# Kernel tuning notes

Measured on AMD Instinct MI355X. Metric: run time of the kernel, lower is better.

## Reference

```python
import jax, jax.numpy as jnp
import numpy as np

N = 50000
E = 800000
IN_DIM = 128
HID = 128
HEADS = 8
OUT_DIM = 64
NEG_SLOPE = 0.2


def setup_inputs() -> dict:
    key = jax.random.key(0)
    ks = jax.random.split(key, 12)
    x = jax.random.normal(ks[0], (N, IN_DIM), dtype=jnp.float32)
    edge_index = jax.random.randint(ks[1], (2, E), 0, N, dtype=jnp.int64)
    C1 = HID // HEADS  # per-head out dim of layer 1
    s1 = 1.0 / np.sqrt(IN_DIM)
    s2 = 1.0 / np.sqrt(HID)
    W1 = jax.random.uniform(ks[2], (IN_DIM, HEADS * C1), jnp.float32, -s1, s1)
    a_src1 = jax.random.uniform(ks[3], (HEADS, C1), jnp.float32, -1.0, 1.0)
    a_dst1 = jax.random.uniform(ks[4], (HEADS, C1), jnp.float32, -1.0, 1.0)
    b1 = jnp.zeros((HEADS * C1,), jnp.float32)
    W2 = jax.random.uniform(ks[5], (HID, OUT_DIM), jnp.float32, -s2, s2)
    a_src2 = jax.random.uniform(ks[6], (1, OUT_DIM), jnp.float32, -1.0, 1.0)
    a_dst2 = jax.random.uniform(ks[7], (1, OUT_DIM), jnp.float32, -1.0, 1.0)
    b2 = jnp.zeros((OUT_DIM,), jnp.float32)
    return {"x": x, "edge_index": edge_index, "W1": W1, "a_src1": a_src1,
            "a_dst1": a_dst1, "b1": b1, "W2": W2, "a_src2": a_src2,
            "a_dst2": a_dst2, "b2": b2}


def gat_conv(x, src, dst, W, a_s, a_d, b, n_heads, c_head):
    # Linear projection per head: [N, H, C]
    h = (x @ W).reshape(N, n_heads, c_head)
    # Per-node attention terms: [N, H]
    alpha_s = jnp.einsum('nhc,hc->nh', h, a_s)
    alpha_d = jnp.einsum('nhc,hc->nh', h, a_d)
    # Per-edge raw scores: [Etot, H]
    score = jax.nn.leaky_relu(alpha_s[src] + alpha_d[dst], negative_slope=NEG_SLOPE)
    # Segment softmax over edges sharing the same destination
    m = jax.ops.segment_max(score, dst, num_segments=N)
    e = jnp.exp(score - m[dst])
    denom = jax.ops.segment_sum(e, dst, num_segments=N)
    alpha = e / denom[dst]  # every node has a self-loop -> denom > 0
    # Weighted aggregation: scatter-add alpha * h_src into destinations
    out = jax.ops.segment_sum(alpha[:, :, None] * h[src], dst, num_segments=N)
    return out.reshape(N, n_heads * c_head) + b


def reference(x, edge_index, W1, a_src1, a_dst1, b1, W2, a_src2, a_dst2, b2):
    # add self loops (GATConv add_self_loops=True)
    loops = jnp.arange(N, dtype=edge_index.dtype)
    src = jnp.concatenate([edge_index[0], loops])
    dst = jnp.concatenate([edge_index[1], loops])
    C1 = HID // HEADS
    h = gat_conv(x, src, dst, W1, a_src1, a_dst1, b1, HEADS, C1)
    h = jax.nn.elu(h)  # dropout = 0 (eval)
    out = gat_conv(h, src, dst, W2, a_src2, a_dst2, b2, 1, OUT_DIM)
    return jax.nn.log_softmax(out, axis=-1)
```

## Files before the change

### kernel.cpp

```cpp
#include <hip/hip_runtime.h>
#include <math.h>

typedef unsigned int  u32;
typedef unsigned short u16;
typedef short bf16x8 __attribute__((ext_vector_type(8)));
typedef float f32x4  __attribute__((ext_vector_type(4)));

#define NN    50000
#define NE    800000
#define ET    (NE + NN)
#define IND   128
#define HIDD  128
#define NH    8
#define OD    64
#define SLOPE 0.2f

#define NB    196
#define EPB   4096
#define NBB   ((NE + EPB - 1) / EPB)
#define LCAP  64
#define CAPB  5120
#define CPAD  16
#define BSTRIDE 7168

#define W1EXT 144
#define W2EXT 80
#define WPB   112
#define G1B   391

__device__ __forceinline__ u32 bf16rne(float f) {
    u32 u = __float_as_uint(f);
    return (u + 0x7fffu + ((u >> 16) & 1u)) >> 16;
}

#define LR(s) fmaxf((s), SLOPE * (s))

__global__ __launch_bounds__(256) void k_prep_bin(
    const int* __restrict__ ei, int* __restrict__ cnt, u32* __restrict__ staging,
    const float* __restrict__ W1, const float* __restrict__ W2,
    const float* __restrict__ as1w, const float* __restrict__ ad1w,
    const float* __restrict__ as2w, const float* __restrict__ ad2w,
    u16* __restrict__ Wt1, u16* __restrict__ Wt2,
    u32* __restrict__ h1b, float* __restrict__ as1, float* __restrict__ as2)
{
    __shared__ u32 lbuf[NB * LCAP];
    __shared__ int lcnt[NB];
    __shared__ int gbase[NB];
    const int t = threadIdx.x;

    if (blockIdx.x >= NBB) {
        const int i = (blockIdx.x - NBB) * 256 + t;
        if (i < 64) h1b[(size_t)64 * NN + i] = 0;
        if (i < 8)  as1[(size_t)NH * NN + i] = -1e30f;
        if (i == 8) as2[NN] = -1e30f;

        if (i < W1EXT * 128) {
            const int j = i >> 7, k = i & 127;
            float v;
            if (j < 128) {
                v = W1[k * 128 + j];
            } else if (j < 136) {
                const int h = j - 128;
                v = 0.f;
                for (int c = 0; c < 16; ++c)
                    v += W1[k * 128 + h * 16 + c] * as1w[h * 16 + c];
            } else {
                const int h = j - 136;
                v = 0.f;
                for (int c = 0; c < 16; ++c)
                    v += W1[k * 128 + h * 16 + c] * ad1w[h * 16 + c];
            }
            Wt1[j * 128 + k] = (u16)bf16rne(v);
        } else if (i < W1EXT * 128 + W2EXT * 128) {
            const int i2 = i - W1EXT * 128;
            const int j = i2 >> 7, k = i2 & 127;
            float v = 0.f;
            if (j < 64) {
                v = W2[k * 64 + j];
            } else if (j == 64) {
                for (int c = 0; c < 64; ++c) v += W2[k * 64 + c] * as2w[c];
            } else if (j == 65) {
                for (int c = 0; c < 64; ++c) v += W2[k * 64 + c] * ad2w[c];
            }
            Wt2[j * 128 + k] = (u16)bf16rne(v);
        }
        return;
    }

    const int e0 = blockIdx.x * EPB;
    for (int i = t; i < NB; i += 256) lcnt[i] = 0;
    __syncthreads();

    for (int i = t; i < EPB; i += 256) {
        const int e = e0 + i;
        if (e >= NE) break;
        const int src = ei[e];
        const int dst = ei[NE + e];
        const int b = dst >> 8;
        const int p = atomicAdd(&lcnt[b], 1);
        lbuf[b * LCAP + p] = ((u32)(dst & 255) << 16) | (u32)src;
    }
    __syncthreads();

    for (int i = t; i < NB; i += 256)
        gbase[i] = atomicAdd(&cnt[i * CPAD], lcnt[i]);
    __syncthreads();

    for (int b = t; b < NB; b += 256) {
        const int n = lcnt[b];
        const int gb = gbase[b];
        u32* dstp = staging + (size_t)b * CAPB + gb;
        const u32* srcp = lbuf + b * LCAP;
        for (int j = 0; j < n; ++j) dstp[j] = srcp[j];
    }
}

__global__ __launch_bounds__(512) void k_place_gemm1(
    const int* __restrict__ cnt, const u32* __restrict__ staging,
    int* __restrict__ rowptr, int* __restrict__ rowend,
    u16* __restrict__ sorted16,
    const float* __restrict__ x, const u16* __restrict__ Wt1,
    u16* __restrict__ h1s, float* __restrict__ as1, float* __restrict__ ad1)
{
    __shared__ u32 xb[128 * 64];
    __shared__ u32 Wb[W1EXT * 64];
    const int tid = threadIdx.x;

    if (blockIdx.x < NB) {
        int* hist = (int*)xb;
        int* cur  = hist + 256;
        int* scan = cur + 256;
        const int b = blockIdx.x;
        const int tot = cnt[b * CPAD];
        const int base = b * BSTRIDE;

        if (tid < 256) hist[tid] = ((b * 256 + tid) < NN) ? 1 : 0;
        __syncthreads();

        for (int i = tid; i < tot; i += 512)
            atomicAdd(&hist[staging[(size_t)b * CAPB + i] >> 16], 1);
        __syncthreads();

        if (tid < 256) scan[tid] = (hist[tid] + 7) & ~7;
        __syncthreads();
        for (int off = 1; off < 256; off <<= 1) {
            int v = 0;
            if (tid < 256 && tid >= off) v = scan[tid - off];
            __syncthreads();
            if (tid < 256) scan[tid] += v;
            __syncthreads();
        }
        if (tid < 256) {
            const int padded = (hist[tid] + 7) & ~7;
            const int excl = (tid == 0) ? 0 : scan[tid - 1];
            const int node = b * 256 + tid;
            if (node < NN) {
                rowptr[node] = base + excl;
                rowend[node] = base + excl + padded;
                sorted16[base + excl] = (u16)node;
                for (int j = hist[tid]; j < padded; ++j)
                    sorted16[base + excl + j] = (u16)NN;
                cur[tid] = excl + 1;
            } else {
                cur[tid] = excl;
            }
        }
        __syncthreads();
        for (int i = tid; i < tot; i += 512) {
            const u32 v = staging[(size_t)b * CAPB + i];
            const int pos = atomicAdd(&cur[v >> 16], 1);
            sorted16[base + pos] = (u16)(v & 0xffffu);
        }
        return;
    }

    const int row0 = (blockIdx.x - NB) * 128;

    {
        const uint4* Wt = (const uint4*)Wt1;
        for (int p = 0; p < 5; ++p) {
            const int id = p * 512 + tid;
            if (id < W1EXT * 16) {
                const int n = id >> 4, c = id & 15;
                *(uint4*)(Wb + n * 64 + ((c ^ (n & 15)) << 2)) = Wt[n * 16 + c];
            }
        }
    }
    for (int p = 0; p < 4; ++p) {
        const int id = p * 512 + tid;
        const int m = id >> 4, c = id & 15;
        const int row = row0 + m;
        uint4 v = make_uint4(0, 0, 0, 0);
        if (row < NN) {
            const float4 f0 = *(const float4*)(x + (size_t)row * 128 + c * 8);
            const float4 f1 = *(const float4*)(x + (size_t)row * 128 + c * 8 + 4);
            v.x = bf16rne(f0.x) | (bf16rne(f0.y) << 16);
            v.y = bf16rne(f0.z) | (bf16rne(f0.w) << 16);
            v.z = bf16rne(f1.x) | (bf16rne(f1.y) << 16);
            v.w = bf16rne(f1.z) | (bf16rne(f1.w) << 16);
        }
        *(uint4*)(xb + m * 64 + ((c ^ (m & 15)) << 2)) = v;
    }
    __syncthreads();

    const int w = tid >> 6, lane = tid & 63;
    const int nl = lane & 15, quad = lane >> 4;
    f32x4 acc[9] = {};
    for (int kk = 0; kk < 4; ++kk) {
        const int cm = kk * 4 + quad;
        const bf16x8 a = *(const bf16x8*)(xb + (16 * w + nl) * 64 + ((cm ^ nl) << 2));
#pragma unroll
        for (int tn = 0; tn < 9; ++tn) {
            const bf16x8 b = *(const bf16x8*)(Wb + (16 * tn + nl) * 64 + ((cm ^ nl) << 2));
            acc[tn] = __builtin_amdgcn_mfma_f32_16x16x32_bf16(a, b, acc[tn], 0, 0, 0);
        }
    }

    __syncthreads();
    {
        u16* h1ld = (u16*)xb;
#pragma unroll
        for (int tn = 0; tn < 8; ++tn) {
#pragma unroll
            for (int r = 0; r < 4; ++r) {
                const int row = 16 * w + quad * 4 + r;
                h1ld[row * 128 + 16 * tn + nl] = (u16)bf16rne(acc[tn][r]);
            }
        }
    }
#pragma unroll
    for (int r = 0; r < 4; ++r) {
        const int row = row0 + 16 * w + quad * 4 + r;
        if (row < NN) {
            const float v = acc[8][r];
            if (nl < 8) as1[row * NH + nl] = v;
            else        ad1[row * NH + (nl - 8)] = v;
        }
    }
    __syncthreads();
    for (int p = 0; p < 4; ++p) {
        const int id = p * 512 + tid;
        const int row = id >> 4, c = id & 15;
        const int grow = row0 + row;
        if (grow < NN)
            ((uint4*)h1s)[(size_t)grow * 16 + c] = ((const uint4*)xb)[row * 16 + c];
    }
}

__global__ __launch_bounds__(512) void k_gemm2(
    const u32* __restrict__ act2b, const u16* __restrict__ Wt2,
    u16* __restrict__ h2s, float* __restrict__ as2, float* __restrict__ ad2)
{
    __shared__ u32 xb[128 * 64];
    __shared__ u32 Wb[W2EXT * 64];
    const int tid = threadIdx.x;
    const int row0 = blockIdx.x * 128;

    {
        const uint4* Wt = (const uint4*)Wt2;
        for (int p = 0; p < 3; ++p) {
            const int id = p * 512 + tid;
            if (id < W2EXT * 16) {
                const int n = id >> 4, c = id & 15;
                *(uint4*)(Wb + n * 64 + ((c ^ (n & 15)) << 2)) = Wt[n * 16 + c];
            }
        }
    }
    for (int p = 0; p < 4; ++p) {
        const int id = p * 512 + tid;
        const int m = id >> 4, c = id & 15;
        const int row = row0 + m;
        uint4 v = make_uint4(0, 0, 0, 0);
        if (row < NN) v = ((const uint4*)act2b)[(size_t)row * 16 + c];
        *(uint4*)(xb + m * 64 + ((c ^ (m & 15)) << 2)) = v;
    }
    __syncthreads();

    const int w = tid >> 6, lane = tid & 63;
    const int nl = lane & 15, quad = lane >> 4;
    f32x4 acc[5] = {};
    for (int kk = 0; kk < 4; ++kk) {
        const int cm = kk * 4 + quad;
        const bf16x8 a = *(const bf16x8*)(xb + (16 * w + nl) * 64 + ((cm ^ nl) << 2));
#pragma unroll
        for (int tn = 0; tn < 5; ++tn) {
            const bf16x8 b = *(const bf16x8*)(Wb + (16 * tn + nl) * 64 + ((cm ^ nl) << 2));
            acc[tn] = __builtin_amdgcn_mfma_f32_16x16x32_bf16(a, b, acc[tn], 0, 0, 0);
        }
    }

    __syncthreads();
    {
        u16* h2ld = (u16*)xb;
#pragma unroll
        for (int tn = 0; tn < 4; ++tn) {
#pragma unroll
            for (int r = 0; r < 4; ++r) {
                const int row = 16 * w + quad * 4 + r;
                h2ld[row * 64 + 16 * tn + nl] = (u16)bf16rne(acc[tn][r]);
            }
        }
    }
#pragma unroll
    for (int r = 0; r < 4; ++r) {
        const int row = row0 + 16 * w + quad * 4 + r;
        if (row < NN) {
            const float v = acc[4][r];
            if (nl == 0) as2[row] = v;
            else if (nl == 1) ad2[row] = v;
        }
    }
    __syncthreads();
    for (int p = 0; p < 2; ++p) {
        const int id = p * 512 + tid;
        const int row = id >> 3, c = id & 7;
        const int grow = row0 + row;
        if (grow < NN)
            ((uint4*)h2s)[(size_t)grow * 8 + c] = ((const uint4*)xb)[row * 8 + c];
    }
}

#define PG1(KK, S, G, WJ) do {                                                \
    const uint4 p = *(const uint4*)(sorted16 + (KK));                         \
    S[0] = p.x & 0xffffu; S[1] = p.x >> 16;                                   \
    S[2] = p.y & 0xffffu; S[3] = p.y >> 16;                                   \
    S[4] = p.z & 0xffffu; S[5] = p.z >> 16;                                   \
    S[6] = p.w & 0xffffu; S[7] = p.w >> 16;                                   \
    const u32 hlf = (head & 4) ? ((head & 2) ? p.w : p.z)                     \
                               : ((head & 2) ? p.y : p.x);                    \
    const u32 sj = (head & 1) ? (hlf >> 16) : (hlf & 0xffffu);                \
    WJ = __expf(LR(as1[sj * NH + eh] + adeh));                                \
    _Pragma("unroll") for (int j = 0; j < 8; ++j)                             \
        G[j] = h1b[S[j] * 64 + lane];                                         \
} while (0)

#define CONS1(G, WJ) do {                                                     \
    _Pragma("unroll") for (int j = 0; j < 8; ++j) {                           \
        const float wv = __uint_as_float((u32)__builtin_amdgcn_ds_bpermute(   \
            h4 + j * 32, (int)__float_as_uint(WJ)));                          \
        acc0 += wv * __uint_as_float(G[j] << 16);                             \
        acc1 += wv * __uint_as_float(G[j] & 0xffff0000u);                     \
        den  += wv; }                                                         \
} while (0)

__global__ __launch_bounds__(256) void k_agg1(
    const int* __restrict__ rowptr, const int* __restrict__ rowend,
    const u16* __restrict__ sorted16,
    const u32* __restrict__ h1b, const float* __restrict__ as1,
    const float* __restrict__ ad1,
    u32* __restrict__ act2b)
{
    const int node = blockIdx.x * 4 + (threadIdx.x >> 6);
    const int lane = threadIdx.x & 63;
    const int head = lane >> 3;
    const int eh   = lane & 7;
    const float adeh = ad1[node * NH + eh];
    const int k0 = rowptr[node], kend = rowend[node];
    const int h4 = head << 2;
    float acc0 = 0.f, acc1 = 0.f, den = 0.f;
    u32 sA[8], gA[8], sB[8], gB[8];
    float wA, wB;

    PG1(k0, sA, gA, wA);
    int k = k0 + 8;
    while (k + 16 <= kend) {
        PG1(k, sB, gB, wB);      CONS1(gA, wA);
        PG1(k + 8, sA, gA, wA);  CONS1(gB, wB);
        k += 16;
    }
    if (k < kend) {
        PG1(k, sB, gB, wB);  CONS1(gA, wA);  CONS1(gB, wB);
    } else {
        CONS1(gA, wA);
    }

    const float inv = 1.f / den;
    float v0 = acc0 * inv, v1 = acc1 * inv;
    v0 = v0 > 0.f ? v0 : expm1f(v0);
    v1 = v1 > 0.f ? v1 : expm1f(v1);
    act2b[node * 64 + lane] = bf16rne(v0) | (bf16rne(v1) << 16);
}

#define PG2(KK, S, G, WJ) do {                                                \
    const uint4 p = *(const uint4*)(sorted16 + (KK));                         \
    S[0] = p.x & 0xffffu; S[1] = p.x >> 16;                                   \
    S[2] = p.y & 0xffffu; S[3] = p.y >> 16;                                   \
    S[4] = p.z & 0xffffu; S[5] = p.z >> 16;                                   \
    S[6] = p.w & 0xffffu; S[7] = p.w >> 16;                                   \
    const u32 hlf = (lane & 4) ? ((lane & 2) ? p.w : p.z)                     \
                               : ((lane & 2) ? p.y : p.x);                    \
    const u32 sj = (lane & 1) ? (hlf >> 16) : (hlf & 0xffffu);                \
    WJ = __expf(LR(as2[sj] + adv));                                           \
    _Pragma("unroll") for (int j = 0; j < 8; ++j)                             \
        G[j] = h2s[S[j] * 64 + lane];                                         \
} while (0)

#define CONS2(G, WJ) do {                                                     \
    _Pragma("unroll") for (int j = 0; j < 8; ++j) {                           \
        const float wv = __uint_as_float((u32)__builtin_amdgcn_ds_bpermute(   \
            j << 2, (int)__float_as_uint(WJ)));                               \
        acc += wv * __uint_as_float(((u32)G[j]) << 16);                       \
        den += wv; }                                                          \
} while (0)

__global__ __launch_bounds__(256) void k_agg2(
    const int* __restrict__ rowptr, const int* __restrict__ rowend,
    const u16* __restrict__ sorted16,
    const u16* __restrict__ h2s, const float* __restrict__ as2,
    const float* __restrict__ ad2,
    float* __restrict__ out)
{
    const int node = blockIdx.x * 4 + (threadIdx.x >> 6);
    const int lane = threadIdx.x & 63;
    const float adv = ad2[node];
    const int k0 = rowptr[node], kend = rowend[node];
    float acc = 0.f, den = 0.f;
    u32 sA[8], gA[8], sB[8], gB[8];
    float wA, wB;

    PG2(k0, sA, gA, wA);
    int k = k0 + 8;
    while (k + 16 <= kend) {
        PG2(k, sB, gB, wB);      CONS2(gA, wA);
        PG2(k + 8, sA, gA, wA);  CONS2(gB, wB);
        k += 16;
    }
    if (k < kend) {
        PG2(k, sB, gB, wB);  CONS2(gA, wA);  CONS2(gB, wB);
    } else {
        CONS2(gA, wA);
    }

    const float v = acc / den;
    float m = v;
    for (int kk = 1; kk < 64; kk <<= 1) m = fmaxf(m, __shfl_xor(m, kk));
    float se = __expf(v - m);
    for (int kk = 1; kk < 64; kk <<= 1) se += __shfl_xor(se, kk);
    out[node * 64 + lane] = v - m - logf(se);
}

extern "C" void kernel_launch(void* const* d_in, const int* in_sizes, int n_in,
                              void* d_out, int out_size, void* d_ws, size_t ws_size,
                              hipStream_t stream)
{
    (void)in_sizes; (void)n_in; (void)out_size; (void)ws_size;
    const float* x    = (const float*)d_in[0];
    const int*   ei   = (const int*)d_in[1];
    const float* W1   = (const float*)d_in[2];
    const float* as1w = (const float*)d_in[3];
    const float* ad1w = (const float*)d_in[4];
    const float* W2   = (const float*)d_in[6];
    const float* as2w = (const float*)d_in[7];
    const float* ad2w = (const float*)d_in[8];
    float* out = (float*)d_out;

    u32* ws = (u32*)d_ws;
    size_t o = 0;
    auto take = [&](size_t n) { size_t r = o; o += (n + 15) & ~(size_t)15; return r; };

    u32*   h1b      = ws + take((size_t)64 * (NN + 1));
    float* as1      = (float*)(ws + take((size_t)NH * NN + 8));
    float* ad1      = (float*)(ws + take((size_t)NH * NN));
    u32*   act2b    = ws + take((size_t)64 * NN);
    float* as2      = (float*)(ws + take(NN + 1));
    float* ad2      = (float*)(ws + take(NN));
    int*   rowptr   = (int*)(ws + take(NN));
    int*   rowend   = (int*)(ws + take(NN));
    u16*   sorted16 = (u16*)(ws + take(((size_t)NB * BSTRIDE + 1) / 2));
    u32*   staging  = ws + take((size_t)NB * CAPB);
    int*   cnt      = (int*)(ws + take(NB * CPAD));
    u16*   Wt1      = (u16*)(ws + take((size_t)W1EXT * 128 / 2));
    u16*   Wt2      = (u16*)(ws + take((size_t)W2EXT * 128 / 2));
    u16*   h1s      = (u16*)h1b;
    u16*   h2s      = (u16*)h1b;

    hipMemsetAsync(cnt, 0, NB * CPAD * sizeof(int), stream);

    k_prep_bin<<<NBB + WPB, 256, 0, stream>>>(
        ei, cnt, staging, W1, W2, as1w, ad1w, as2w, ad2w,
        Wt1, Wt2, h1b, as1, as2);

    k_place_gemm1<<<NB + G1B, 512, 0, stream>>>(
        cnt, staging, rowptr, rowend, sorted16, x, Wt1, h1s, as1, ad1);

    k_agg1<<<NN / 4, 256, 0, stream>>>(rowptr, rowend, sorted16, h1b, as1, ad1, act2b);
    k_gemm2<<<G1B, 512, 0, stream>>>(act2b, Wt2, h2s, as2, ad2);
    k_agg2<<<NN / 4, 256, 0, stream>>>(rowptr, rowend, sorted16, h2s, as2, ad2, out);
}
```

Before: 183.5 us.

## Gather feature rows with 16-byte vector loads split across lane groups in aggregation

Both aggregation kernels change how source feature rows are gathered. Before, each lane loaded one 32-bit word per edge for eight edges. Now each lane loads a 16-byte chunk of a row, so one wavefront gathers several edges' rows at once (2 edges per pass in layer 1, 8 in layer 2). Partial sums are then combined across lane groups with xor-shuffles, and the output is written by a subset of lanes using vector stores. The aim is fewer, wider memory instructions and fewer bpermutes per edge, at the cost of extra cross-lane reductions and more accumulator registers.

```diff
diff --git a/kernel.cpp b/kernel.cpp
--- a/kernel.cpp
+++ b/kernel.cpp
@@ -34,6 +34,13 @@
 }
 
 #define LR(s) fmaxf((s), SLOPE * (s))
+
+__device__ __forceinline__ u32 sel8(uint4 p, int e) {
+    const u32 c = (e & 4) ? ((e & 2) ? p.w : p.z) : ((e & 2) ? p.y : p.x);
+    return (e & 1) ? (c >> 16) : (c & 0xffffu);
+}
+#define BFLO(u) __uint_as_float((u) << 16)
+#define BFHI(u) __uint_as_float((u) & 0xffff0000u)
 
 __global__ __launch_bounds__(256) void k_prep_bin(
     const int* __restrict__ ei, int* __restrict__ cnt, u32* __restrict__ staging,
@@ -320,33 +327,36 @@
     }
 }
 
-#define PG1(KK, S, G, WJ) do {                                                \
-    const uint4 p = *(const uint4*)(sorted16 + (KK));                         \
-    S[0] = p.x & 0xffffu; S[1] = p.x >> 16;                                   \
-    S[2] = p.y & 0xffffu; S[3] = p.y >> 16;                                   \
-    S[4] = p.z & 0xffffu; S[5] = p.z >> 16;                                   \
-    S[6] = p.w & 0xffffu; S[7] = p.w >> 16;                                   \
-    const u32 hlf = (head & 4) ? ((head & 2) ? p.w : p.z)                     \
-                               : ((head & 2) ? p.y : p.x);                    \
-    const u32 sj = (head & 1) ? (hlf >> 16) : (hlf & 0xffffu);                \
+#define PG1(KK, P, G0, G1, WJ) do {                                           \
+    P = *(const uint4*)(sorted16 + (KK));                                     \
+    const u32 sj = sel8(P, head);                                             \
     WJ = __expf(LR(as1[sj * NH + eh] + adeh));                                \
-    _Pragma("unroll") for (int j = 0; j < 8; ++j)                             \
-        G[j] = h1b[S[j] * 64 + lane];                                         \
+    const u32 s0 = sel8(P, esel);                                             \
+    const u32 s1 = sel8(P, 4 + esel);                                         \
+    G0 = *(const uint4*)(h1g + (size_t)s0 * 128 + ch8);                       \
+    G1 = *(const uint4*)(h1g + (size_t)s1 * 128 + ch8);                       \
 } while (0)
 
-#define CONS1(G, WJ) do {                                                     \
-    _Pragma("unroll") for (int j = 0; j < 8; ++j) {                           \
-        const float wv = __uint_as_float((u32)__builtin_amdgcn_ds_bpermute(   \
-            h4 + j * 32, (int)__float_as_uint(WJ)));                          \
-        acc0 += wv * __uint_as_float(G[j] << 16);                             \
-        acc1 += wv * __uint_as_float(G[j] & 0xffff0000u);                     \
-        den  += wv; }                                                         \
+#define CONS1(G0, G1, WJ) do {                                                \
+    const float w0 = __uint_as_float((u32)__builtin_amdgcn_ds_bpermute(       \
+        bp0, (int)__float_as_uint(WJ)));                                      \
+    const float w1 = __uint_as_float((u32)__builtin_amdgcn_ds_bpermute(       \
+        bp1, (int)__float_as_uint(WJ)));                                      \
+    acc[0] += w0 * BFLO(G0.x); acc[1] += w0 * BFHI(G0.x);                     \
+    acc[2] += w0 * BFLO(G0.y); acc[3] += w0 * BFHI(G0.y);                     \
+    acc[4] += w0 * BFLO(G0.z); acc[5] += w0 * BFHI(G0.z);                     \
+    acc[6] += w0 * BFLO(G0.w); acc[7] += w0 * BFHI(G0.w);                     \
+    acc[0] += w1 * BFLO(G1.x); acc[1] += w1 * BFHI(G1.x);                     \
+    acc[2] += w1 * BFLO(G1.y); acc[3] += w1 * BFHI(G1.y);                     \
+    acc[4] += w1 * BFLO(G1.z); acc[5] += w1 * BFHI(G1.z);                     \
+    acc[6] += w1 * BFLO(G1.w); acc[7] += w1 * BFHI(G1.w);                     \
+    den += w0 + w1;                                                           \
 } while (0)
 
 __global__ __launch_bounds__(256) void k_agg1(
     const int* __restrict__ rowptr, const int* __restrict__ rowend,
     const u16* __restrict__ sorted16,
-    const u32* __restrict__ h1b, const float* __restrict__ as1,
+    const u16* __restrict__ h1g, const float* __restrict__ as1,
     const float* __restrict__ ad1,
     u32* __restrict__ act2b)
 {
@@ -355,88 +365,134 @@
     const int head = lane >> 3;
     const int eh   = lane & 7;
     const float adeh = ad1[node * NH + eh];
+    const int esel = lane >> 4;
+    const int ch8  = (lane & 15) * 8;
+    const int mh   = (lane & 15) >> 1;
+    const int bp0  = (esel * 8 + mh) << 2;
+    const int bp1  = bp0 + 128;
     const int k0 = rowptr[node], kend = rowend[node];
-    const int h4 = head << 2;
-    float acc0 = 0.f, acc1 = 0.f, den = 0.f;
-    u32 sA[8], gA[8], sB[8], gB[8];
+    float acc[8] = {0.f, 0.f, 0.f, 0.f, 0.f, 0.f, 0.f, 0.f};
+    float den = 0.f;
+    uint4 pA, gA0, gA1, pB, gB0, gB1;
     float wA, wB;
 
-    PG1(k0, sA, gA, wA);
+    PG1(k0, pA, gA0, gA1, wA);
     int k = k0 + 8;
     while (k + 16 <= kend) {
-        PG1(k, sB, gB, wB);      CONS1(gA, wA);
-        PG1(k + 8, sA, gA, wA);  CONS1(gB, wB);
+        PG1(k, pB, gB0, gB1, wB);        CONS1(gA0, gA1, wA);
+        PG1(k + 8, pA, gA0, gA1, wA);    CONS1(gB0, gB1, wB);
         k += 16;
     }
     if (k < kend) {
-        PG1(k, sB, gB, wB);  CONS1(gA, wA);  CONS1(gB, wB);
+        PG1(k, pB, gB0, gB1, wB);  CONS1(gA0, gA1, wA);  CONS1(gB0, gB1, wB);
     } else {
-        CONS1(gA, wA);
-    }
+        CONS1(gA0, gA1, wA);
+    }
+
+#pragma unroll
+    for (int i = 0; i < 8; ++i) {
+        acc[i] += __shfl_xor(acc[i], 16);
+        acc[i] += __shfl_xor(acc[i], 32);
+    }
+    den += __shfl_xor(den, 16);
+    den += __shfl_xor(den, 32);
 
     const float inv = 1.f / den;
-    float v0 = acc0 * inv, v1 = acc1 * inv;
-    v0 = v0 > 0.f ? v0 : expm1f(v0);
-    v1 = v1 > 0.f ? v1 : expm1f(v1);
-    act2b[node * 64 + lane] = bf16rne(v0) | (bf16rne(v1) << 16);
-}
-
-#define PG2(KK, S, G, WJ) do {                                                \
-    const uint4 p = *(const uint4*)(sorted16 + (KK));                         \
-    S[0] = p.x & 0xffffu; S[1] = p.x >> 16;                                   \
-    S[2] = p.y & 0xffffu; S[3] = p.y >> 16;                                   \
-    S[4] = p.z & 0xffffu; S[5] = p.z >> 16;                                   \
-    S[6] = p.w & 0xffffu; S[7] = p.w >> 16;                                   \
-    const u32 hlf = (lane & 4) ? ((lane & 2) ? p.w : p.z)                     \
-                               : ((lane & 2) ? p.y : p.x);                    \
-    const u32 sj = (lane & 1) ? (hlf >> 16) : (hlf & 0xffffu);                \
+    u32 o[4];
+#pragma unroll
+    for (int i = 0; i < 4; ++i) {
+        float v0 = acc[2 * i] * inv, v1 = acc[2 * i + 1] * inv;
+        v0 = v0 > 0.f ? v0 : expm1f(v0);
+        v1 = v1 > 0.f ? v1 : expm1f(v1);
+        o[i] = bf16rne(v0) | (bf16rne(v1) << 16);
+    }
+    if (lane < 16)
+        *(uint4*)(act2b + (size_t)node * 64 + lane * 4) =
+            make_uint4(o[0], o[1], o[2], o[3]);
+}
+
+#define PG2(KK, P, G, WJ) do {                                                \
+    P = *(const uint4*)(sorted16 + (KK));                                     \
+    const u32 sj = sel8(P, eh2);                                              \
     WJ = __expf(LR(as2[sj] + adv));                                           \
-    _Pragma("unroll") for (int j = 0; j < 8; ++j)                             \
-        G[j] = h2s[S[j] * 64 + lane];                                         \
+    const u32 s = sel8(P, es2);                                               \
+    G = *(const uint4*)(h2g + (size_t)s * 64 + ch8b);                         \
 } while (0)
 
 #define CONS2(G, WJ) do {                                                     \
-    _Pragma("unroll") for (int j = 0; j < 8; ++j) {                           \
-        const float wv = __uint_as_float((u32)__builtin_amdgcn_ds_bpermute(   \
-            j << 2, (int)__float_as_uint(WJ)));                               \
-        acc += wv * __uint_as_float(((u32)G[j]) << 16);                       \
-        den += wv; }                                                          \
+    const float wv = __uint_as_float((u32)__builtin_amdgcn_ds_bpermute(       \
+        bpa, (int)__float_as_uint(WJ)));                                      \
+    acc[0] += wv * BFLO(G.x); acc[1] += wv * BFHI(G.x);                       \
+    acc[2] += wv * BFLO(G.y); acc[3] += wv * BFHI(G.y);                       \
+    acc[4] += wv * BFLO(G.z); acc[5] += wv * BFHI(G.z);                       \
+    acc[6] += wv * BFLO(G.w); acc[7] += wv * BFHI(G.w);                       \
+    den += wv;                                                                \
 } while (0)
 
 __global__ __launch_bounds__(256) void k_agg2(
     const int* __restrict__ rowptr, const int* __restrict__ rowend,
     const u16* __restrict__ sorted16,
-    const u16* __restrict__ h2s, const float* __restrict__ as2,
+    const u16* __restrict__ h2g, const float* __restrict__ as2,
     const float* __restrict__ ad2,
     float* __restrict__ out)
 {
     const int node = blockIdx.x * 4 + (threadIdx.x >> 6);
     const int lane = threadIdx.x & 63;
     const float adv = ad2[node];
+    const int eh2  = lane & 7;
+    const int es2  = lane >> 3;
+    const int ch8b = (lane & 7) * 8;
+    const int bpa  = es2 << 2;
     const int k0 = rowptr[node], kend = rowend[node];
-    float acc = 0.f, den = 0.f;
-    u32 sA[8], gA[8], sB[8], gB[8];
+    float acc[8] = {0.f, 0.f, 0.f, 0.f, 0.f, 0.f, 0.f, 0.f};
+    float den = 0.f;
+    uint4 pA, gA, pB, gB;
     float wA, wB;
 
-    PG2(k0, sA, gA, wA);
+    PG2(k0, pA, gA, wA);
     int k = k0 + 8;
     while (k + 16 <= kend) {
-        PG2(k, sB, gB, wB);      CONS2(gA, wA);
-        PG2(k + 8, sA, gA, wA);  CONS2(gB, wB);
+        PG2(k, pB, gB, wB);      CONS2(gA, wA);
+        PG2(k + 8, pA, gA, wA);  CONS2(gB, wB);
         k += 16;
     }
     if (k < kend) {
-        PG2(k, sB, gB, wB);  CONS2(gA, wA);  CONS2(gB, wB);
+        PG2(k, pB, gB, wB);  CONS2(gA, wA);  CONS2(gB, wB);
     } else {
         CONS2(gA, wA);
     }
 
-    const float v = acc / den;
-    float m = v;
-    for (int kk = 1; kk < 64; kk <<= 1) m = fmaxf(m, __shfl_xor(m, kk));
-    float se = __expf(v - m);
-    for (int kk = 1; kk < 64; kk <<= 1) se += __shfl_xor(se, kk);
-    out[node * 64 + lane] = v - m - logf(se);
+#pragma unroll
+    for (int i = 0; i < 8; ++i) {
+        acc[i] += __shfl_xor(acc[i], 8);
+        acc[i] += __shfl_xor(acc[i], 16);
+        acc[i] += __shfl_xor(acc[i], 32);
+    }
+    den += __shfl_xor(den, 8);
+    den += __shfl_xor(den, 16);
+    den += __shfl_xor(den, 32);
+
+    const float inv = 1.f / den;
+    float v[8];
+    float m = -1e30f;
+#pragma unroll
+    for (int i = 0; i < 8; ++i) { v[i] = acc[i] * inv; m = fmaxf(m, v[i]); }
+    m = fmaxf(m, __shfl_xor(m, 1));
+    m = fmaxf(m, __shfl_xor(m, 2));
+    m = fmaxf(m, __shfl_xor(m, 4));
+    float se = 0.f;
+#pragma unroll
+    for (int i = 0; i < 8; ++i) se += __expf(v[i] - m);
+    se += __shfl_xor(se, 1);
+    se += __shfl_xor(se, 2);
+    se += __shfl_xor(se, 4);
+    const float lse = m + logf(se);
+    if (lane < 8) {
+        float4 o0 = make_float4(v[0] - lse, v[1] - lse, v[2] - lse, v[3] - lse);
+        float4 o1 = make_float4(v[4] - lse, v[5] - lse, v[6] - lse, v[7] - lse);
+        *(float4*)(out + (size_t)node * 64 + lane * 8)     = o0;
+        *(float4*)(out + (size_t)node * 64 + lane * 8 + 4) = o1;
+    }
 }
 
 extern "C" void kernel_launch(void* const* d_in, const int* in_sizes, int n_in,
@@ -483,7 +539,7 @@
     k_place_gemm1<<<NB + G1B, 512, 0, stream>>>(
         cnt, staging, rowptr, rowend, sorted16, x, Wt1, h1s, as1, ad1);
 
-    k_agg1<<<NN / 4, 256, 0, stream>>>(rowptr, rowend, sorted16, h1b, as1, ad1, act2b);
+    k_agg1<<<NN / 4, 256, 0, stream>>>(rowptr, rowend, sorted16, h1s, as1, ad1, act2b);
     k_gemm2<<<G1B, 512, 0, stream>>>(act2b, Wt2, h2s, as2, ad2);
     k_agg2<<<NN / 4, 256, 0, stream>>>(rowptr, rowend, sorted16, h2s, as2, ad2, out);
 }
```

After: 190.3 us. +3.7%, slower.

## Split layer-1 features into head-pair slices for L2-local gather aggregation

Applied to the files above, without the earlier changes.

Stores layer-1 projected features and attention logits in four slice-major planes of two heads each. Aggregation then runs one block per node-quad per slice, so each block gathers a smaller working set. Each lane loads a 16-byte chunk for one of 16 edges and partial sums are reduced with cross-lane shuffles. Row padding grows to 16 entries to match the wider edge step. This aims to improve cache locality of the random gathers, at the cost of four times as many blocks, redundant index reads and extra padding work.

```diff
diff --git a/kernel.cpp b/kernel.cpp
--- a/kernel.cpp
+++ b/kernel.cpp
@@ -21,19 +21,30 @@
 #define LCAP  64
 #define CAPB  5120
 #define CPAD  16
-#define BSTRIDE 7168
+#define BSTRIDE 8192
 
 #define W1EXT 144
 #define W2EXT 80
 #define WPB   112
 #define G1B   391
 
+#define SL_ROW  16
+#define SL_STR  ((size_t)(NN + 1) * SL_ROW)
+#define PSTR    ((size_t)(NN + 1) * 2)
+
 __device__ __forceinline__ u32 bf16rne(float f) {
     u32 u = __float_as_uint(f);
     return (u + 0x7fffu + ((u >> 16) & 1u)) >> 16;
 }
 
 #define LR(s) fmaxf((s), SLOPE * (s))
+
+__device__ __forceinline__ u32 sel8(uint4 p, int e) {
+    const u32 c = (e & 4) ? ((e & 2) ? p.w : p.z) : ((e & 2) ? p.y : p.x);
+    return (e & 1) ? (c >> 16) : (c & 0xffffu);
+}
+#define BFLO(u) __uint_as_float((u) << 16)
+#define BFHI(u) __uint_as_float((u) & 0xffff0000u)
 
 __global__ __launch_bounds__(256) void k_prep_bin(
     const int* __restrict__ ei, int* __restrict__ cnt, u32* __restrict__ staging,
@@ -41,7 +52,7 @@
     const float* __restrict__ as1w, const float* __restrict__ ad1w,
     const float* __restrict__ as2w, const float* __restrict__ ad2w,
     u16* __restrict__ Wt1, u16* __restrict__ Wt2,
-    u32* __restrict__ h1b, float* __restrict__ as1, float* __restrict__ as2)
+    u32* __restrict__ h1sl, float* __restrict__ as1p, float* __restrict__ as2)
 {
     __shared__ u32 lbuf[NB * LCAP];
     __shared__ int lcnt[NB];
@@ -50,8 +61,10 @@
 
     if (blockIdx.x >= NBB) {
         const int i = (blockIdx.x - NBB) * 256 + t;
-        if (i < 64) h1b[(size_t)64 * NN + i] = 0;
-        if (i < 8)  as1[(size_t)NH * NN + i] = -1e30f;
+        if (i < 64)
+            h1sl[(size_t)(i >> 4) * SL_STR + (size_t)NN * SL_ROW + (i & 15)] = 0;
+        if (i < 8)
+            as1p[(size_t)(i >> 1) * PSTR + (size_t)NN * 2 + (i & 1)] = -1e30f;
         if (i == 8) as2[NN] = -1e30f;
 
         if (i < W1EXT * 128) {
@@ -120,7 +133,7 @@
     int* __restrict__ rowptr, int* __restrict__ rowend,
     u16* __restrict__ sorted16,
     const float* __restrict__ x, const u16* __restrict__ Wt1,
-    u16* __restrict__ h1s, float* __restrict__ as1, float* __restrict__ ad1)
+    u32* __restrict__ h1sl, float* __restrict__ as1p, float* __restrict__ ad1p)
 {
     __shared__ u32 xb[128 * 64];
     __shared__ u32 Wb[W1EXT * 64];
@@ -141,7 +154,7 @@
             atomicAdd(&hist[staging[(size_t)b * CAPB + i] >> 16], 1);
         __syncthreads();
 
-        if (tid < 256) scan[tid] = (hist[tid] + 7) & ~7;
+        if (tid < 256) scan[tid] = (hist[tid] + 15) & ~15;
         __syncthreads();
         for (int off = 1; off < 256; off <<= 1) {
             int v = 0;
@@ -151,7 +164,7 @@
             __syncthreads();
         }
         if (tid < 256) {
-            const int padded = (hist[tid] + 7) & ~7;
+            const int padded = (hist[tid] + 15) & ~15;
             const int excl = (tid == 0) ? 0 : scan[tid - 1];
             const int node = b * 256 + tid;
             if (node < NN) {
@@ -233,8 +246,10 @@
         const int row = row0 + 16 * w + quad * 4 + r;
         if (row < NN) {
             const float v = acc[8][r];
-            if (nl < 8) as1[row * NH + nl] = v;
-            else        ad1[row * NH + (nl - 8)] = v;
+            if (nl < 8)
+                as1p[(size_t)(nl >> 1) * PSTR + (size_t)row * 2 + (nl & 1)] = v;
+            else
+                ad1p[(size_t)((nl - 8) >> 1) * PSTR + (size_t)row * 2 + (nl & 1)] = v;
         }
     }
     __syncthreads();
@@ -243,7 +258,8 @@
         const int row = id >> 4, c = id & 15;
         const int grow = row0 + row;
         if (grow < NN)
-            ((uint4*)h1s)[(size_t)grow * 16 + c] = ((const uint4*)xb)[row * 16 + c];
+            ((uint4*)h1sl)[(size_t)(c >> 2) * (NN + 1) * 4 + (size_t)grow * 4 + (c & 3)]
+                = ((const uint4*)xb)[row * 16 + c];
     }
 }
 
@@ -320,65 +336,87 @@
     }
 }
 
-#define PG1(KK, S, G, WJ) do {                                                \
-    const uint4 p = *(const uint4*)(sorted16 + (KK));                         \
-    S[0] = p.x & 0xffffu; S[1] = p.x >> 16;                                   \
-    S[2] = p.y & 0xffffu; S[3] = p.y >> 16;                                   \
-    S[4] = p.z & 0xffffu; S[5] = p.z >> 16;                                   \
-    S[6] = p.w & 0xffffu; S[7] = p.w >> 16;                                   \
-    const u32 hlf = (head & 4) ? ((head & 2) ? p.w : p.z)                     \
-                               : ((head & 2) ? p.y : p.x);                    \
-    const u32 sj = (head & 1) ? (hlf >> 16) : (hlf & 0xffffu);                \
-    WJ = __expf(LR(as1[sj * NH + eh] + adeh));                                \
-    _Pragma("unroll") for (int j = 0; j < 8; ++j)                             \
-        G[j] = h1b[S[j] * 64 + lane];                                         \
+#define PG1(KK, G, W) do {                                                    \
+    const u32 sg_ = sorted16[(KK) + eg];                                      \
+    const u32 se_ = sorted16[(KK) + ee];                                      \
+    const float as_ = asl[(size_t)se_ * 2 + hh];                              \
+    W = __expf(LR(as_ + adv));                                                \
+    G = h1q[(size_t)sg_ * 4 + c4];                                            \
 } while (0)
 
-#define CONS1(G, WJ) do {                                                     \
-    _Pragma("unroll") for (int j = 0; j < 8; ++j) {                           \
-        const float wv = __uint_as_float((u32)__builtin_amdgcn_ds_bpermute(   \
-            h4 + j * 32, (int)__float_as_uint(WJ)));                          \
-        acc0 += wv * __uint_as_float(G[j] << 16);                             \
-        acc1 += wv * __uint_as_float(G[j] & 0xffff0000u);                     \
-        den  += wv; }                                                         \
+#define CONS1(G, W) do {                                                      \
+    const float wv = __uint_as_float((u32)__builtin_amdgcn_ds_bpermute(       \
+        bpa, (int)__float_as_uint(W)));                                       \
+    acc[0] += wv * BFLO(G.x); acc[1] += wv * BFHI(G.x);                       \
+    acc[2] += wv * BFLO(G.y); acc[3] += wv * BFHI(G.y);                       \
+    acc[4] += wv * BFLO(G.z); acc[5] += wv * BFHI(G.z);                       \
+    acc[6] += wv * BFLO(G.w); acc[7] += wv * BFHI(G.w);                       \
+    den += wv;                                                                \
 } while (0)
 
 __global__ __launch_bounds__(256) void k_agg1(
     const int* __restrict__ rowptr, const int* __restrict__ rowend,
     const u16* __restrict__ sorted16,
-    const u32* __restrict__ h1b, const float* __restrict__ as1,
-    const float* __restrict__ ad1,
+    const u32* __restrict__ h1sl, const float* __restrict__ as1p,
+    const float* __restrict__ ad1p,
     u32* __restrict__ act2b)
 {
-    const int node = blockIdx.x * 4 + (threadIdx.x >> 6);
+    const int b = blockIdx.x;
+    const int slice = (b >> 1) & 3;
+    const int nq = (b >> 3) * 2 + (b & 1);
+    const int node = nq * 4 + (threadIdx.x >> 6);
     const int lane = threadIdx.x & 63;
-    const int head = lane >> 3;
-    const int eh   = lane & 7;
-    const float adeh = ad1[node * NH + eh];
+    const int eg = lane >> 2;
+    const int c4 = lane & 3;
+    const int ee = (lane >> 1) & 15;
+    const int hh = lane & 1;
+    const int bpa = ((eg << 1) | ((lane >> 1) & 1)) << 2;
+    const float* asl = as1p + (size_t)slice * PSTR;
+    const float adv = ad1p[(size_t)slice * PSTR + (size_t)node * 2 + hh];
+    const uint4* h1q = (const uint4*)h1sl + (size_t)slice * (NN + 1) * 4;
     const int k0 = rowptr[node], kend = rowend[node];
-    const int h4 = head << 2;
-    float acc0 = 0.f, acc1 = 0.f, den = 0.f;
-    u32 sA[8], gA[8], sB[8], gB[8];
+    float acc[8] = {0.f, 0.f, 0.f, 0.f, 0.f, 0.f, 0.f, 0.f};
+    float den = 0.f;
+    uint4 gA, gB;
     float wA, wB;
 
-    PG1(k0, sA, gA, wA);
-    int k = k0 + 8;
-    while (k + 16 <= kend) {
-        PG1(k, sB, gB, wB);      CONS1(gA, wA);
-        PG1(k + 8, sA, gA, wA);  CONS1(gB, wB);
-        k += 16;
+    PG1(k0, gA, wA);
+    int k = k0 + 16;
+    while (k + 32 <= kend) {
+        PG1(k, gB, wB);       CONS1(gA, wA);
+        PG1(k + 16, gA, wA);  CONS1(gB, wB);
+        k += 32;
     }
     if (k < kend) {
-        PG1(k, sB, gB, wB);  CONS1(gA, wA);  CONS1(gB, wB);
+        PG1(k, gB, wB);  CONS1(gA, wA);  CONS1(gB, wB);
     } else {
         CONS1(gA, wA);
     }
 
+#pragma unroll
+    for (int i = 0; i < 8; ++i) {
+        acc[i] += __shfl_xor(acc[i], 4);
+        acc[i] += __shfl_xor(acc[i], 8);
+        acc[i] += __shfl_xor(acc[i], 16);
+        acc[i] += __shfl_xor(acc[i], 32);
+    }
+    den += __shfl_xor(den, 4);
+    den += __shfl_xor(den, 8);
+    den += __shfl_xor(den, 16);
+    den += __shfl_xor(den, 32);
+
     const float inv = 1.f / den;
-    float v0 = acc0 * inv, v1 = acc1 * inv;
-    v0 = v0 > 0.f ? v0 : expm1f(v0);
-    v1 = v1 > 0.f ? v1 : expm1f(v1);
-    act2b[node * 64 + lane] = bf16rne(v0) | (bf16rne(v1) << 16);
+    u32 o[4];
+#pragma unroll
+    for (int i = 0; i < 4; ++i) {
+        float v0 = acc[2 * i] * inv, v1 = acc[2 * i + 1] * inv;
+        v0 = v0 > 0.f ? v0 : expm1f(v0);
+        v1 = v1 > 0.f ? v1 : expm1f(v1);
+        o[i] = bf16rne(v0) | (bf16rne(v1) << 16);
+    }
+    if (lane < 4)
+        *(uint4*)(act2b + (size_t)node * 64 + slice * 16 + lane * 4) =
+            make_uint4(o[0], o[1], o[2], o[3]);
 }
 
 #define PG2(KK, S, G, WJ) do {                                                \
@@ -387,9 +425,7 @@
     S[2] = p.y & 0xffffu; S[3] = p.y >> 16;                                   \
     S[4] = p.z & 0xffffu; S[5] = p.z >> 16;                                   \
     S[6] = p.w & 0xffffu; S[7] = p.w >> 16;                                   \
-    const u32 hlf = (lane & 4) ? ((lane & 2) ? p.w : p.z)                     \
-                               : ((lane & 2) ? p.y : p.x);                    \
-    const u32 sj = (lane & 1) ? (hlf >> 16) : (hlf & 0xffffu);                \
+    const u32 sj = sel8(p, lane & 7);                                         \
     WJ = __expf(LR(as2[sj] + adv));                                           \
     _Pragma("unroll") for (int j = 0; j < 8; ++j)                             \
         G[j] = h2s[S[j] * 64 + lane];                                         \
@@ -458,9 +494,9 @@
     size_t o = 0;
     auto take = [&](size_t n) { size_t r = o; o += (n + 15) & ~(size_t)15; return r; };
 
-    u32*   h1b      = ws + take((size_t)64 * (NN + 1));
-    float* as1      = (float*)(ws + take((size_t)NH * NN + 8));
-    float* ad1      = (float*)(ws + take((size_t)NH * NN));
+    u32*   h1sl     = ws + take(4 * SL_STR);
+    float* as1p     = (float*)(ws + take(4 * PSTR));
+    float* ad1p     = (float*)(ws + take(4 * PSTR));
     u32*   act2b    = ws + take((size_t)64 * NN);
     float* as2      = (float*)(ws + take(NN + 1));
     float* ad2      = (float*)(ws + take(NN));
@@ -471,19 +507,18 @@
     int*   cnt      = (int*)(ws + take(NB * CPAD));
     u16*   Wt1      = (u16*)(ws + take((size_t)W1EXT * 128 / 2));
     u16*   Wt2      = (u16*)(ws + take((size_t)W2EXT * 128 / 2));
-    u16*   h1s      = (u16*)h1b;
-    u16*   h2s      = (u16*)h1b;
+    u16*   h2s      = (u16*)h1sl;
 
     hipMemsetAsync(cnt, 0, NB * CPAD * sizeof(int), stream);
 
     k_prep_bin<<<NBB + WPB, 256, 0, stream>>>(
         ei, cnt, staging, W1, W2, as1w, ad1w, as2w, ad2w,
-        Wt1, Wt2, h1b, as1, as2);
+        Wt1, Wt2, h1sl, as1p, as2);
 
     k_place_gemm1<<<NB + G1B, 512, 0, stream>>>(
-        cnt, staging, rowptr, rowend, sorted16, x, Wt1, h1s, as1, ad1);
-
-    k_agg1<<<NN / 4, 256, 0, stream>>>(rowptr, rowend, sorted16, h1b, as1, ad1, act2b);
+        cnt, staging, rowptr, rowend, sorted16, x, Wt1, h1sl, as1p, ad1p);
+
+    k_agg1<<<NN, 256, 0, stream>>>(rowptr, rowend, sorted16, h1sl, as1p, ad1p, act2b);
     k_gemm2<<<G1B, 512, 0, stream>>>(act2b, Wt2, h2s, as2, ad2);
     k_agg2<<<NN / 4, 256, 0, stream>>>(rowptr, rowend, sorted16, h2s, as2, ad2, out);
 }
```

Result: slower. 254.1 us (+38.5%).
